# Kernel optimization log

Hardware: AMD Instinct MI355X
Metric: run time of the kernel (lower is better)

The kernel has to match this reference:

```python
import jax, jax.numpy as jnp
import numpy as np

N, E, D, H = 50000, 800000, 256, 256
EPS = 1e-12


def _sage_pool(h, src, dst, W_pool, b_pool, W_self, W_neigh, b):
    # DGL SAGEConv aggregator_type='pool':
    #   m = relu(fc_pool(h_src)); h_neigh = max over in-neighbors; 
    #   out = fc_self(h_dst) + fc_neigh(h_neigh) + bias
    m = jax.nn.relu(h @ W_pool + b_pool)                # [N, D]
    msgs = m[src]                                        # [E, D] irregular gather
    agg = jax.ops.segment_max(msgs, dst, num_segments=N)  # [N, D]
    agg = jnp.where(jnp.isfinite(agg), agg, 0.0)         # zero-in-degree -> 0
    return h @ W_self + agg @ W_neigh + b


def _l2norm(h):
    # torch F.normalize(dim=1)
    n = jnp.linalg.norm(h, axis=1, keepdims=True)
    return h / jnp.maximum(n, EPS)


def setup_inputs() -> dict:
    key = jax.random.key(0)
    ks = jax.random.split(key, 13)
    s = 1.0 / np.sqrt(D)
    inp = {
        "x": jax.random.normal(ks[0], (N, D), jnp.float32),
        "src": jax.random.randint(ks[1], (E,), 0, N, jnp.int32),
        "dst": jax.random.randint(ks[2], (E,), 0, N, jnp.int32),
        "W_pool0": jax.random.normal(ks[3], (D, D), jnp.float32) * s,
        "b_pool0": jnp.zeros((D,), jnp.float32),
        "W_self0": jax.random.normal(ks[4], (D, H), jnp.float32) * s,
        "W_neigh0": jax.random.normal(ks[5], (D, H), jnp.float32) * s,
        "b0": jnp.zeros((H,), jnp.float32),
        "W_pool1": jax.random.normal(ks[6], (H, H), jnp.float32) * s,
        "b_pool1": jnp.zeros((H,), jnp.float32),
        "W_self1": jax.random.normal(ks[7], (H, H), jnp.float32) * s,
        "W_neigh1": jax.random.normal(ks[8], (H, H), jnp.float32) * s,
        "b1": jnp.zeros((H,), jnp.float32),
    }
    return inp


def reference(x, src, dst, W_pool0, b_pool0, W_self0, W_neigh0, b0,
              W_pool1, b_pool1, W_self1, W_neigh1, b1):
    # layer 0: conv -> relu -> l2-normalize -> dropout (identity at eval)
    h = _sage_pool(x, src, dst, W_pool0, b_pool0, W_self0, W_neigh0, b0)
    h = _l2norm(jax.nn.relu(h))
    enc_feat_input = h
    # layer 1 (last): conv only
    h = _sage_pool(h, src, dst, W_pool1, b_pool1, W_self1, W_neigh1, b1)
    return (h, enc_feat_input)
```

## Files before the change

kernel.cpp:

```cpp
#include <hip/hip_runtime.h>
#include <cstddef>

#define D256 256

typedef __attribute__((ext_vector_type(8))) short bf16x8;
typedef __attribute__((ext_vector_type(4))) float f32x4;

#define GLOAD16(gptr, lptr)                                                         \
    __builtin_amdgcn_global_load_lds(                                               \
        (const __attribute__((address_space(1))) unsigned int*)(gptr),              \
        (__attribute__((address_space(3))) unsigned int*)(lptr), 16, 0, 0)

__device__ __forceinline__ ushort f2bf(float f) {
    unsigned u = __float_as_uint(f);
    return (ushort)((u + 0x7FFFu + ((u >> 16) & 1u)) >> 16);
}
__device__ __forceinline__ ushort umax16(ushort a, ushort b) { return a > b ? a : b; }
__device__ __forceinline__ ushort4 vmax4(ushort4 a, ushort4 b) {
    return make_ushort4(umax16(a.x, b.x), umax16(a.y, b.y),
                        umax16(a.z, b.z), umax16(a.w, b.w));
}

template<int DUAL, int RELU, int OUT_BF16>
__global__ __launch_bounds__(256)
void mfma_gemm_kernel(const ushort* __restrict__ A, const ushort* __restrict__ Bt,
                      const ushort* __restrict__ A2, const ushort* __restrict__ Bt2,
                      const float* __restrict__ bias, void* __restrict__ outp, int M)
{
    constexpr int TILES = DUAL ? 4 : 2;
    constexpr int BUFSZ = TILES * 4096;
    __shared__ ushort smem[2 * BUFSZ];

    const int t    = threadIdx.x;
    const int m0   = blockIdx.x * 128;
    const int n0   = blockIdx.y * 128;
    const int lane = t & 63;
    const int wave = t >> 6;
    const int wr   = (wave >> 1) * 64;
    const int wc   = (wave & 1) * 64;
    const int lr   = lane & 15;
    const int kg   = lane >> 4;

    const int lrow  = lane >> 2;
    const int lch   = lane & 3;
    const int srow0 = wave * 32;

    f32x4 acc[4][4];
#pragma unroll
    for (int i = 0; i < 4; ++i)
#pragma unroll
        for (int j = 0; j < 4; ++j) acc[i][j] = (f32x4)(0.0f);

    auto STAGE = [&](int buf, int k0) {
        ushort* const base = smem + buf * BUFSZ;
#pragma unroll
        for (int i = 0; i < 2; ++i) {
            const int r   = srow0 + i * 16;
            const int ar  = m0 + r + lrow;
            const int arc = ar < M ? ar : (M - 1);
            const size_t ga = (size_t)arc * D256 + k0 + lch * 8;
            const size_t gb = (size_t)(n0 + r + lrow) * D256 + k0 + lch * 8;
            GLOAD16(A + ga, base + r * 32);
            GLOAD16(Bt + gb, base + 4096 + r * 32);
            if (DUAL) {
                GLOAD16(A2 + ga, base + 8192 + r * 32);
                GLOAD16(Bt2 + gb, base + 12288 + r * 32);
            }
        }
    };

    STAGE(0, 0);
#pragma unroll
    for (int ks = 0; ks < 8; ++ks) {
        const int cur = ks & 1;
        __syncthreads();
        if (ks < 7) STAGE(cur ^ 1, (ks + 1) * 32);

        ushort* const base = smem + cur * BUFSZ;
        bf16x8 af[4], bf[4];
#pragma unroll
        for (int mi = 0; mi < 4; ++mi)
            af[mi] = *(const bf16x8*)&base[(wr + mi * 16 + lr) * 32 + kg * 8];
#pragma unroll
        for (int ni = 0; ni < 4; ++ni)
            bf[ni] = *(const bf16x8*)&base[4096 + (wc + ni * 16 + lr) * 32 + kg * 8];
#pragma unroll
        for (int mi = 0; mi < 4; ++mi)
#pragma unroll
            for (int ni = 0; ni < 4; ++ni)
                acc[mi][ni] = __builtin_amdgcn_mfma_f32_16x16x32_bf16(
                    bf[ni], af[mi], acc[mi][ni], 0, 0, 0);
        if (DUAL) {
            bf16x8 af2[4], bf2[4];
#pragma unroll
            for (int mi = 0; mi < 4; ++mi)
                af2[mi] = *(const bf16x8*)&base[8192 + (wr + mi * 16 + lr) * 32 + kg * 8];
#pragma unroll
            for (int ni = 0; ni < 4; ++ni)
                bf2[ni] = *(const bf16x8*)&base[12288 + (wc + ni * 16 + lr) * 32 + kg * 8];
#pragma unroll
            for (int mi = 0; mi < 4; ++mi)
#pragma unroll
                for (int ni = 0; ni < 4; ++ni)
                    acc[mi][ni] = __builtin_amdgcn_mfma_f32_16x16x32_bf16(
                        bf2[ni], af2[mi], acc[mi][ni], 0, 0, 0);
        }
    }

#pragma unroll
    for (int ni = 0; ni < 4; ++ni) {
        const int colb = n0 + wc + ni * 16 + kg * 4;
        const float4 bb = *(const float4*)(bias + colb);
#pragma unroll
        for (int mi = 0; mi < 4; ++mi) {
            const int row = m0 + wr + mi * 16 + lr;
            if (row < M) {
                const f32x4 a = acc[mi][ni];
                float4 o;
                o.x = a[0] + bb.x;
                o.y = a[1] + bb.y;
                o.z = a[2] + bb.z;
                o.w = a[3] + bb.w;
                if (RELU) {
                    o.x = fmaxf(o.x, 0.f); o.y = fmaxf(o.y, 0.f);
                    o.z = fmaxf(o.z, 0.f); o.w = fmaxf(o.w, 0.f);
                }
                if (OUT_BF16) {
                    ushort4 ob;
                    ob.x = f2bf(o.x); ob.y = f2bf(o.y);
                    ob.z = f2bf(o.z); ob.w = f2bf(o.w);
                    *(ushort4*)((ushort*)outp + (size_t)row * D256 + colb) = ob;
                } else {
                    *(float4*)((float*)outp + (size_t)row * D256 + colb) = o;
                }
            }
        }
    }
}

__global__ __launch_bounds__(256)
void f2bf_kernel(const float* __restrict__ in, ushort* __restrict__ out, int n4)
{
    const int i = blockIdx.x * 256 + threadIdx.x;
    if (i >= n4) return;
    const float4 v = ((const float4*)in)[i];
    ushort4 o;
    o.x = f2bf(v.x); o.y = f2bf(v.y); o.z = f2bf(v.z); o.w = f2bf(v.w);
    ((ushort4*)out)[i] = o;
}

struct WP  { const float* w; ushort* o; };
struct WP6 { WP p[6]; };
__global__ __launch_bounds__(256)
void wtrans_kernel(WP6 ps)
{
    const float* __restrict__ W = ps.p[blockIdx.z].w;
    ushort* __restrict__ O      = ps.p[blockIdx.z].o;
    __shared__ float sm[32][33];
    const int tx = threadIdx.x & 31, ty = threadIdx.x >> 5;
    const int k0 = blockIdx.x * 32, n0 = blockIdx.y * 32;
#pragma unroll
    for (int i = 0; i < 4; ++i)
        sm[ty + i * 8][tx] = W[(size_t)(k0 + ty + i * 8) * D256 + n0 + tx];
    __syncthreads();
#pragma unroll
    for (int i = 0; i < 4; ++i)
        O[(size_t)(n0 + ty + i * 8) * D256 + k0 + tx] = f2bf(sm[tx][ty + i * 8]);
}

__global__ __launch_bounds__(256)
void hist_kernel(const int* __restrict__ dst, int* __restrict__ deg, int E)
{
    const int stride = gridDim.x * 256;
    for (int e = blockIdx.x * 256 + threadIdx.x; e < E; e += stride)
        atomicAdd(&deg[dst[e]], 1);
}

__global__ __launch_bounds__(1024)
void blockscan_kernel(const int* __restrict__ deg, int* __restrict__ incl,
                      int* __restrict__ partials, int N)
{
    __shared__ int wt[16];
    const int i    = blockIdx.x * 1024 + threadIdx.x;
    const int lane = threadIdx.x & 63;
    const int wv   = threadIdx.x >> 6;
    const int v    = (i < N) ? deg[i] : 0;
    int s = v;
#pragma unroll
    for (int o = 1; o < 64; o <<= 1) {
        const int t = __shfl_up(s, o);
        if (lane >= o) s += t;
    }
    if (lane == 63) wt[wv] = s;
    __syncthreads();
    if (wv == 0 && lane < 16) {
        const int w = wt[lane];
        int ws = w;
#pragma unroll
        for (int o = 1; o < 16; o <<= 1) {
            const int t = __shfl_up(ws, o);
            if (lane >= o) ws += t;
        }
        wt[lane] = ws - w;
    }
    __syncthreads();
    s += wt[wv];
    if (i < N) incl[i] = s;
    if (threadIdx.x == 1023) partials[blockIdx.x] = s;
}

__global__ __launch_bounds__(1024)
void scanp_kernel(int* __restrict__ partials, int nb)
{
    __shared__ int sm[1024];
    const int v = (threadIdx.x < (unsigned)nb) ? partials[threadIdx.x] : 0;
    sm[threadIdx.x] = v;
    __syncthreads();
#pragma unroll
    for (int off = 1; off < 1024; off <<= 1) {
        const int t = (threadIdx.x >= (unsigned)off) ? sm[threadIdx.x - off] : 0;
        __syncthreads();
        sm[threadIdx.x] += t;
        __syncthreads();
    }
    if (threadIdx.x < (unsigned)nb) partials[threadIdx.x] = sm[threadIdx.x] - v;
}

__global__ __launch_bounds__(1024)
void finalize_kernel(const int* __restrict__ deg, const int* __restrict__ incl,
                     const int* __restrict__ partials, int* __restrict__ row_ptr,
                     int* __restrict__ cursor, int N, int E)
{
    const int i = blockIdx.x * 1024 + threadIdx.x;
    if (i < N) {
        const int ex = partials[blockIdx.x] + incl[i] - deg[i];
        row_ptr[i] = ex;
        cursor[i]  = ex;
    }
    if (i == 0) row_ptr[N] = E;
}

__global__ __launch_bounds__(256)
void bucket_kernel(const int* __restrict__ src, const int* __restrict__ dst,
                   int* __restrict__ cursor, int* __restrict__ esrc, int E)
{
    const int stride = gridDim.x * 256;
    for (int e = blockIdx.x * 256 + threadIdx.x; e < E; e += stride) {
        const int p = atomicAdd(&cursor[dst[e]], 1);
        esrc[p] = src[e];
    }
}

__global__ __launch_bounds__(256)
void agg_max_kernel(const int* __restrict__ row_ptr, const int* __restrict__ esrc,
                    const ushort* __restrict__ m, ushort* __restrict__ agg, int N)
{
    const int wid  = (int)(((size_t)blockIdx.x * 256 + threadIdx.x) >> 6);
    const int lane = threadIdx.x & 63;
    if (wid >= N) return;
    const int beg = row_ptr[wid];
    const int end = row_ptr[wid + 1];
    const size_t off = (size_t)(lane * 4);

    ushort4 a0 = make_ushort4(0, 0, 0, 0);
    ushort4 a1 = a0, a2 = a0, a3 = a0;
    int e = beg;
    for (; e + 8 <= end; e += 8) {
        int s[8];
#pragma unroll
        for (int q = 0; q < 8; ++q) s[q] = esrc[e + q];
        ushort4 v[8];
#pragma unroll
        for (int q = 0; q < 8; ++q)
            v[q] = *(const ushort4*)(m + (size_t)s[q] * D256 + off);
        a0 = vmax4(a0, vmax4(v[0], v[4]));
        a1 = vmax4(a1, vmax4(v[1], v[5]));
        a2 = vmax4(a2, vmax4(v[2], v[6]));
        a3 = vmax4(a3, vmax4(v[3], v[7]));
    }
    for (; e + 2 <= end; e += 2) {
        const int s0 = esrc[e];
        const int s1 = esrc[e + 1];
        const ushort4 v0 = *(const ushort4*)(m + (size_t)s0 * D256 + off);
        const ushort4 v1 = *(const ushort4*)(m + (size_t)s1 * D256 + off);
        a0 = vmax4(a0, v0);
        a1 = vmax4(a1, v1);
    }
    if (e < end) {
        const ushort4 v0 = *(const ushort4*)(m + (size_t)esrc[e] * D256 + off);
        a2 = vmax4(a2, v0);
    }
    const ushort4 r = vmax4(vmax4(a0, a1), vmax4(a2, a3));
    *(ushort4*)(agg + (size_t)wid * D256 + off) = r;
}

__global__ __launch_bounds__(256)
void l2norm_kernel(const float* __restrict__ in, float* __restrict__ out_f,
                   ushort* __restrict__ out_b, int M)
{
    const int wid  = (int)(((size_t)blockIdx.x * 256 + threadIdx.x) >> 6);
    const int lane = threadIdx.x & 63;
    if (wid >= M) return;
    const float4 v = *(const float4*)(in + (size_t)wid * D256 + lane * 4);
    float ss = v.x * v.x + v.y * v.y + v.z * v.z + v.w * v.w;
#pragma unroll
    for (int o = 32; o >= 1; o >>= 1) ss += __shfl_xor(ss, o);
    const float inv = 1.0f / fmaxf(sqrtf(ss), 1e-12f);
    float4 o4;
    o4.x = v.x * inv; o4.y = v.y * inv; o4.z = v.z * inv; o4.w = v.w * inv;
    *(float4*)(out_f + (size_t)wid * D256 + lane * 4) = o4;
    ushort4 ob;
    ob.x = f2bf(o4.x); ob.y = f2bf(o4.y); ob.z = f2bf(o4.z); ob.w = f2bf(o4.w);
    *(ushort4*)(out_b + (size_t)wid * D256 + lane * 4) = ob;
}

extern "C" void kernel_launch(void* const* d_in, const int* in_sizes, int n_in,
                              void* d_out, int out_size, void* d_ws, size_t ws_size,
                              hipStream_t stream)
{
    const float* x        = (const float*)d_in[0];
    const int*   src      = (const int*)  d_in[1];
    const int*   dst      = (const int*)  d_in[2];
    const float* W_pool0  = (const float*)d_in[3];
    const float* b_pool0  = (const float*)d_in[4];
    const float* W_self0  = (const float*)d_in[5];
    const float* W_neigh0 = (const float*)d_in[6];
    const float* b0       = (const float*)d_in[7];
    const float* W_pool1  = (const float*)d_in[8];
    const float* b_pool1  = (const float*)d_in[9];
    const float* W_self1  = (const float*)d_in[10];
    const float* W_neigh1 = (const float*)d_in[11];
    const float* b1       = (const float*)d_in[12];

    const int N = in_sizes[0] / D256;
    const int E = in_sizes[1];
    const size_t NR = (size_t)N * D256;

    float* h1  = (float*)d_out;
    float* enc = (float*)d_out + NR;

    ushort* xb   = (ushort*)d_ws;
    ushort* mb   = xb + NR;
    ushort* aggb = mb + NR;
    float*  tmp  = (float*)(aggb + NR);
    ushort* Bt   = (ushort*)(tmp + NR);
    int* row_ptr = (int*)(Bt + 6 * 256 * 256);
    int* cursor  = row_ptr + (N + 1);
    int* deg     = cursor + N;
    int* incl    = deg + N;
    int* partials= incl + N;
    int* esrc    = partials + 1024;

    ushort* Bt_pool0  = Bt + 0 * 65536;
    ushort* Bt_self0  = Bt + 1 * 65536;
    ushort* Bt_neigh0 = Bt + 2 * 65536;
    ushort* Bt_pool1  = Bt + 3 * 65536;
    ushort* Bt_self1  = Bt + 4 * 65536;
    ushort* Bt_neigh1 = Bt + 5 * 65536;

    const dim3 gemm_grid((N + 127) / 128, 2);
    const int  edge_blocks = (E + 255) / 256 < 2048 ? (E + 255) / 256 : 2048;
    const int  node_blocks = (N + 3) / 4;
    const int  conv_blocks = (int)((NR / 4 + 255) / 256);
    const int  scan_blocks = (N + 1023) / 1024;

    WP6 wp;
    wp.p[0] = { W_pool0,  Bt_pool0  };
    wp.p[1] = { W_self0,  Bt_self0  };
    wp.p[2] = { W_neigh0, Bt_neigh0 };
    wp.p[3] = { W_pool1,  Bt_pool1  };
    wp.p[4] = { W_self1,  Bt_self1  };
    wp.p[5] = { W_neigh1, Bt_neigh1 };
    wtrans_kernel<<<dim3(8, 8, 6), 256, 0, stream>>>(wp);
    f2bf_kernel<<<conv_blocks, 256, 0, stream>>>(x, xb, (int)(NR / 4));

    hipMemsetAsync(deg, 0, (size_t)N * sizeof(int), stream);
    hist_kernel<<<edge_blocks, 256, 0, stream>>>(dst, deg, E);
    blockscan_kernel<<<scan_blocks, 1024, 0, stream>>>(deg, incl, partials, N);
    scanp_kernel<<<1, 1024, 0, stream>>>(partials, scan_blocks);
    finalize_kernel<<<scan_blocks, 1024, 0, stream>>>(deg, incl, partials,
                                                      row_ptr, cursor, N, E);
    bucket_kernel<<<edge_blocks, 256, 0, stream>>>(src, dst, cursor, esrc, E);

    mfma_gemm_kernel<0,1,1><<<gemm_grid, 256, 0, stream>>>(xb, Bt_pool0, nullptr, nullptr,
                                                           b_pool0, mb, N);
    agg_max_kernel<<<node_blocks, 256, 0, stream>>>(row_ptr, esrc, mb, aggb, N);
    mfma_gemm_kernel<1,1,0><<<gemm_grid, 256, 0, stream>>>(xb, Bt_self0, aggb, Bt_neigh0,
                                                           b0, tmp, N);
    l2norm_kernel<<<node_blocks, 256, 0, stream>>>(tmp, enc, xb, N);

    mfma_gemm_kernel<0,1,1><<<gemm_grid, 256, 0, stream>>>(xb, Bt_pool1, nullptr, nullptr,
                                                           b_pool1, mb, N);
    agg_max_kernel<<<node_blocks, 256, 0, stream>>>(row_ptr, esrc, mb, aggb, N);
    mfma_gemm_kernel<1,0,0><<<gemm_grid, 256, 0, stream>>>(xb, Bt_self1, aggb, Bt_neigh1,
                                                           b1, h1, N);
}
```

Before: 375.8 us.

## Switch max aggregation to thread-per-node with feature slices across grid y

Replaces the wave-per-node max aggregation with a kernel where each thread handles one destination node and a 32-feature slice, with eight slices spread over the grid's y dimension. Each thread walks its CSR neighbor list and does an elementwise max over a contiguous 64-byte chunk of each source row. This is meant to increase parallelism and cut per-wave index overhead. In exchange, lanes in a wave read different random rows with no coalescing, and neighbor-count imbalance within a wave causes divergence.

Measured after the change: 509.6 us. 35.6% more time.

```diff
diff --git a/kernel.cpp b/kernel.cpp
--- a/kernel.cpp
+++ b/kernel.cpp
@@ -252,46 +252,32 @@
 }
 
 __global__ __launch_bounds__(256)
-void agg_max_kernel(const int* __restrict__ row_ptr, const int* __restrict__ esrc,
-                    const ushort* __restrict__ m, ushort* __restrict__ agg, int N)
-{
-    const int wid  = (int)(((size_t)blockIdx.x * 256 + threadIdx.x) >> 6);
-    const int lane = threadIdx.x & 63;
-    if (wid >= N) return;
-    const int beg = row_ptr[wid];
-    const int end = row_ptr[wid + 1];
-    const size_t off = (size_t)(lane * 4);
-
-    ushort4 a0 = make_ushort4(0, 0, 0, 0);
-    ushort4 a1 = a0, a2 = a0, a3 = a0;
-    int e = beg;
-    for (; e + 8 <= end; e += 8) {
-        int s[8];
-#pragma unroll
-        for (int q = 0; q < 8; ++q) s[q] = esrc[e + q];
-        ushort4 v[8];
-#pragma unroll
-        for (int q = 0; q < 8; ++q)
-            v[q] = *(const ushort4*)(m + (size_t)s[q] * D256 + off);
-        a0 = vmax4(a0, vmax4(v[0], v[4]));
-        a1 = vmax4(a1, vmax4(v[1], v[5]));
-        a2 = vmax4(a2, vmax4(v[2], v[6]));
-        a3 = vmax4(a3, vmax4(v[3], v[7]));
-    }
-    for (; e + 2 <= end; e += 2) {
-        const int s0 = esrc[e];
-        const int s1 = esrc[e + 1];
-        const ushort4 v0 = *(const ushort4*)(m + (size_t)s0 * D256 + off);
-        const ushort4 v1 = *(const ushort4*)(m + (size_t)s1 * D256 + off);
-        a0 = vmax4(a0, v0);
-        a1 = vmax4(a1, v1);
-    }
-    if (e < end) {
-        const ushort4 v0 = *(const ushort4*)(m + (size_t)esrc[e] * D256 + off);
-        a2 = vmax4(a2, v0);
-    }
-    const ushort4 r = vmax4(vmax4(a0, a1), vmax4(a2, a3));
-    *(ushort4*)(agg + (size_t)wid * D256 + off) = r;
+void agg_max_tslice_kernel(const int* __restrict__ row_ptr, const int* __restrict__ esrc,
+                           const ushort* __restrict__ m, ushort* __restrict__ agg, int N)
+{
+    const int node  = blockIdx.x * 256 + threadIdx.x;
+    const int slice = blockIdx.y;
+    if (node >= N) return;
+    const int beg = row_ptr[node];
+    const int end = row_ptr[node + 1];
+    const ushort* __restrict__ ms = m + slice * 32;
+
+    ushort4 a[8];
+#pragma unroll
+    for (int j = 0; j < 8; ++j) a[j] = make_ushort4(0, 0, 0, 0);
+
+    for (int e = beg; e < end; ++e) {
+        const int s = esrc[e];
+        const ushort* __restrict__ row = ms + (size_t)s * D256;
+#pragma unroll
+        for (int j = 0; j < 8; ++j)
+            a[j] = vmax4(a[j], *(const ushort4*)(row + j * 4));
+    }
+
+    ushort* __restrict__ out = agg + (size_t)node * D256 + slice * 32;
+#pragma unroll
+    for (int j = 0; j < 8; ++j)
+        *(ushort4*)(out + j * 4) = a[j];
 }
 
 __global__ __launch_bounds__(256)
@@ -363,6 +349,7 @@
     const int  node_blocks = (N + 3) / 4;
     const int  conv_blocks = (int)((NR / 4 + 255) / 256);
     const int  scan_blocks = (N + 1023) / 1024;
+    const dim3 agg_grid((N + 255) / 256, 8);
 
     WP6 wp;
     wp.p[0] = { W_pool0,  Bt_pool0  };
@@ -384,14 +371,14 @@
 
     mfma_gemm_kernel<0,1,1><<<gemm_grid, 256, 0, stream>>>(xb, Bt_pool0, nullptr, nullptr,
                                                            b_pool0, mb, N);
-    agg_max_kernel<<<node_blocks, 256, 0, stream>>>(row_ptr, esrc, mb, aggb, N);
+    agg_max_tslice_kernel<<<agg_grid, 256, 0, stream>>>(row_ptr, esrc, mb, aggb, N);
     mfma_gemm_kernel<1,1,0><<<gemm_grid, 256, 0, stream>>>(xb, Bt_self0, aggb, Bt_neigh0,
                                                            b0, tmp, N);
     l2norm_kernel<<<node_blocks, 256, 0, stream>>>(tmp, enc, xb, N);
 
     mfma_gemm_kernel<0,1,1><<<gemm_grid, 256, 0, stream>>>(xb, Bt_pool1, nullptr, nullptr,
                                                            b_pool1, mb, N);
-    agg_max_kernel<<<node_blocks, 256, 0, stream>>>(row_ptr, esrc, mb, aggb, N);
+    agg_max_tslice_kernel<<<agg_grid, 256, 0, stream>>>(row_ptr, esrc, mb, aggb, N);
     mfma_gemm_kernel<1,0,0><<<gemm_grid, 256, 0, stream>>>(xb, Bt_self1, aggb, Bt_neigh1,
                                                            b1, h1, N);
 }
```
